# Kernel tuning notes

Hardware: AMD Instinct MI355X
Metric: run time of the kernel (lower is better)

## Reference

```python
import jax, jax.numpy as jnp
import numpy as np

L, B, T, SA, ST = 6, 32, 256, 512, 128
D, H, HD, DFF, OUT = 1024, 16, 64, 4096, 3
ROPE_THETA = 10000.0

def setup_inputs() -> dict:
    key = jax.random.key(0)
    ks = jax.random.split(key, 24)
    w = lambda k, shape: jax.random.normal(k, shape, jnp.float32) * 0.02
    inp = {
        'x':    jax.random.normal(ks[0], (B, T, D), jnp.float32),
        'cond': jax.random.normal(ks[1], (B, D), jnp.float32),
        'adp':  jax.random.normal(ks[2], (B, SA, D), jnp.float32),
        'task': jax.random.normal(ks[3], (B, ST, D), jnp.float32),
        'Wq':  w(ks[4], (L, D, D)),  'bq': jnp.zeros((L, D)),
        'Wks': w(ks[5], (L, D, D)),  'Wvs': w(ks[6], (L, D, D)),
        'Wka': w(ks[7], (L, D, D)),  'Wva': w(ks[8], (L, D, D)),
        'Wkt': w(ks[9], (L, D, D)),  'Wvt': w(ks[10], (L, D, D)),
        'Wo':  w(ks[11], (L, D, D)), 'bo': jnp.zeros((L, D)),
        'qnw': jnp.ones((L, HD)),    'knw': jnp.ones((L, HD)),
        'gate': jnp.zeros((L,)),
        'Wada': w(ks[12], (L, D, 6 * D)), 'bada': jnp.zeros((L, 6 * D)),
        'W1': w(ks[13], (L, D, DFF)), 'b1': jnp.zeros((L, DFF)),
        'W2': w(ks[14], (L, DFF, D)), 'b2': jnp.zeros((L, D)),
        'lnf_w': jnp.ones((D,)), 'lnf_b': jnp.zeros((D,)),
        'Wout': w(ks[15], (D, OUT)), 'bout': jnp.zeros((OUT,)),
    }
    return inp

def _ln(x, eps=1e-5):
    m = x.mean(-1, keepdims=True)
    v = ((x - m) ** 2).mean(-1, keepdims=True)
    return (x - m) * jax.lax.rsqrt(v + eps)

def _rms(x, wgt, eps=1e-6):
    return x * jax.lax.rsqrt((x * x).mean(-1, keepdims=True) + eps) * wgt

def _rotate_half(x):
    h = x.shape[-1] // 2
    return jnp.concatenate([-x[..., h:], x[..., :h]], axis=-1)

def _rope(x, cos, sin):
    # x: (B,S,H,HD); cos/sin: (S,1,HD)
    return x * cos + _rotate_half(x) * sin

def _cos_sin(S):
    inv = 1.0 / (ROPE_THETA ** (jnp.arange(0, HD, 2, dtype=jnp.float32) / HD))
    f = jnp.arange(S, dtype=jnp.float32)[:, None] * inv[None, :]
    emb = jnp.concatenate([f, f], axis=-1)  # (S, HD)
    return jnp.cos(emb)[:, None, :], jnp.sin(emb)[:, None, :]

def _forward(x, cond, adp, task, Wq, bq, Wks, Wvs, Wka, Wva, Wkt, Wvt, Wo, bo,
             qnw, knw, gate, Wada, bada, W1, b1, W2, b2, lnf_w, lnf_b, Wout, bout):
    cosT, sinT = _cos_sin(T)
    cosA, sinA = _cos_sin(SA)
    cosK, sinK = _cos_sin(ST)
    scale = 1.0 / jnp.sqrt(jnp.float32(HD))
    heads = lambda t, W: (t @ W).reshape(t.shape[0], t.shape[1], H, HD)
    for i in range(L):
        ada = jax.nn.silu(cond) @ Wada[i] + bada[i]
        s1, sc1, g1, s2, sc2, g2 = jnp.split(ada, 6, axis=-1)  # each (B,D)
        h = _ln(x) * (1.0 + sc1[:, None]) + s1[:, None]
        # self source: RoPE on Q and K; cross sources: RoPE on K only
        q = _rope(_rms(heads(h, Wq[i]) + bq[i].reshape(H, HD), qnw[i]), cosT, sinT)
        k_s = _rope(_rms(heads(h, Wks[i]), knw[i]), cosT, sinT)
        v_s = heads(h, Wvs[i])
        k_a = _rope(_rms(heads(adp, Wka[i]), knw[i]), cosA, sinA)
        v_a = heads(adp, Wva[i])
        k_t = _rope(_rms(heads(task, Wkt[i]), knw[i]), cosK, sinK)
        v_t = heads(task, Wvt[i])
        ss = jnp.einsum('bthd,bshd->bhts', q, k_s) * scale
        sa = jnp.einsum('bthd,bshd->bhts', q, k_a) * scale
        st = jnp.einsum('bthd,bshd->bhts', q, k_t) * scale * jax.nn.sigmoid(gate[i])
        attn = jax.nn.softmax(jnp.concatenate([ss, sa, st], axis=-1), axis=-1)
        v = jnp.concatenate([v_s, v_a, v_t], axis=1)  # (B, T+SA+ST, H, HD)
        o = jnp.einsum('bhts,bshd->bthd', attn, v).reshape(x.shape[0], T, D)
        x = x + g1[:, None] * (o @ Wo[i] + bo[i])
        h2 = _ln(x) * (1.0 + sc2[:, None]) + s2[:, None]
        ff = jax.nn.gelu(h2 @ W1[i] + b1[i]) @ W2[i] + b2[i]
        x = x + g2[:, None] * ff
    y = _ln(x) * lnf_w + lnf_b
    return y @ Wout + bout

def reference(x, cond, adp, task, Wq, bq, Wks, Wvs, Wka, Wva, Wkt, Wvt, Wo, bo,
              qnw, knw, gate, Wada, bada, W1, b1, W2, b2, lnf_w, lnf_b, Wout, bout):
    return _forward(x, cond, adp, task, Wq, bq, Wks, Wvs, Wka, Wva, Wkt, Wvt, Wo, bo,
                    qnw, knw, gate, Wada, bada, W1, b1, W2, b2, lnf_w, lnf_b, Wout, bout)
```

## Files before the change

kernel.cpp:

```cpp
#include <hip/hip_runtime.h>
#include <stdint.h>

#define DEV static __device__ __forceinline__

#define BB 32
#define TT 256
#define SAA 512
#define STT 128
#define DD 1024
#define HH 16
#define HDD 64
#define DFFF 4096
#define SS 896
#define LL 6

using bf16x8 = __attribute__((ext_vector_type(8))) short;
using f32x4  = __attribute__((ext_vector_type(4))) float;

DEV uint16_t f2bf(float f){
  uint32_t u = __float_as_uint(f);
  uint32_t r = (u + 0x7fffu + ((u >> 16) & 1u)) >> 16;
  return (uint16_t)r;
}
DEV float bf2f(uint16_t b){ return __uint_as_float(((uint32_t)b) << 16); }

typedef __attribute__((address_space(3))) void lds_vt;
typedef __attribute__((address_space(1))) void glb_vt;

DEV void gl_lds16(const uint16_t* g, uint16_t* l){
  __builtin_amdgcn_global_load_lds((const glb_vt*)g, (lds_vt*)l, 16, 0, 0);
}

struct GemmP {
  const uint16_t* A; const uint16_t* B; const uint16_t* B1; const uint16_t* B2;
  uint16_t* outB; float* outF; const float* bias; const float* gvec;
  const float* gatep; float* xres;
  long aOuter, aInner, bOuter, bInner;
  int M, N, K, lda, ldb, ldc, segStart, bShift;
};

template<int MODE>
__global__ __launch_bounds__(256, 2)
void gemm_nt(GemmP p){
  __shared__ uint16_t As[8192];
  __shared__ uint16_t Bs[8192];
  const int tid = threadIdx.x;
  const int w = tid >> 6, l = tid & 63;
  const int n0 = blockIdx.x * 128, m0 = blockIdx.y * 128;

  const uint16_t* Ab = p.A;
  const uint16_t* Bb = p.B + (long)n0 * p.ldb;

  const int rloc = l >> 3, ps = l & 7;
  const int kg_st = (ps - rloc) & 7;

  f32x4 acc[4][4];
  const f32x4 z4 = {0.f, 0.f, 0.f, 0.f};
  #pragma unroll
  for (int a = 0; a < 4; ++a)
    #pragma unroll
    for (int b = 0; b < 4; ++b) acc[a][b] = z4;

  const int KT = p.K >> 6;
  for (int kt = 0; kt < KT; ++kt){
    if (kt) __syncthreads();
    const long kbase = ((long)kt << 6) + (kg_st << 3);
    #pragma unroll
    for (int i = 0; i < 4; ++i){
      const int c = (w << 2) + i;
      int ar = m0 + (c << 3) + rloc;
      if (ar >= p.M) ar = p.M - 1;
      gl_lds16(Ab + (long)ar * p.lda + kbase, &As[c << 9]);
      const int br = (c << 3) + rloc;
      gl_lds16(Bb + (long)br * p.ldb + kbase, &Bs[c << 9]);
    }
    __syncthreads();
    #pragma unroll
    for (int ks = 0; ks < 2; ++ks){
      bf16x8 af[4], bfr[4];
      const int kq = (ks << 2) + (l >> 4);
      #pragma unroll
      for (int mt = 0; mt < 4; ++mt){
        const int r = ((w & 1) << 6) + (mt << 4) + (l & 15);
        af[mt] = *(const bf16x8*)&As[(r << 6) + (((kq + r) & 7) << 3)];
      }
      #pragma unroll
      for (int nt = 0; nt < 4; ++nt){
        const int r = ((w >> 1) << 6) + (nt << 4) + (l & 15);
        bfr[nt] = *(const bf16x8*)&Bs[(r << 6) + (((kq + r) & 7) << 3)];
      }
      #pragma unroll
      for (int mt = 0; mt < 4; ++mt)
        #pragma unroll
        for (int nt = 0; nt < 4; ++nt)
          acc[mt][nt] = __builtin_amdgcn_mfma_f32_16x16x32_bf16(af[mt], bfr[nt], acc[mt][nt], 0, 0, 0);
    }
  }

  const int colb = ((w >> 1) << 6) + (l & 15);
  const int rowb = m0 + ((w & 1) << 6) + ((l >> 4) << 2);
  #pragma unroll
  for (int mt = 0; mt < 4; ++mt){
    #pragma unroll
    for (int nt = 0; nt < 4; ++nt){
      const int col = n0 + colb + (nt << 4);
      const int row0 = rowb + (mt << 4);
      if (MODE == 6){
        const int b = row0 >> p.bShift;
        const int s = row0 & ((1 << p.bShift) - 1);
        const int hh = col >> 6, d = col & 63;
        ushort4 hv;
        hv.x = f2bf(acc[mt][nt][0]); hv.y = f2bf(acc[mt][nt][1]);
        hv.z = f2bf(acc[mt][nt][2]); hv.w = f2bf(acc[mt][nt][3]);
        *(ushort4*)(p.outB + ((long)((b << 4) + hh) * 128 + d) * 896 + p.segStart + s) = hv;
        continue;
      }
      #pragma unroll
      for (int e = 0; e < 4; ++e){
        const int row = row0 + e;
        if (row >= p.M) continue;
        float v = acc[mt][nt][e];
        if (MODE == 0){
          if (p.bias) v += p.bias[col];
          p.outB[(long)row * p.ldc + col] = f2bf(v);
        } else if (MODE == 5){
          v += p.bias[col];
          p.outF[(long)row * p.ldc + col] = v;
        } else if (MODE == 1){
          v += p.bias[col];
          const int b = row >> 8;
          const float g = p.gvec[b * 6144 + col];
          p.xres[(long)row * 1024 + col] += g * v;
        } else if (MODE == 2){
          v += p.bias[col];
          const float u = 0.7978845608028654f * (v + 0.044715f * v * v * v);
          v = 0.5f * v * (1.f + tanhf(u));
          p.outB[(long)row * 4096 + col] = f2bf(v);
        }
      }
    }
  }
}

__global__ __launch_bounds__(256, 2)
void k_attn(const uint16_t* __restrict__ qb, const uint16_t* __restrict__ ksb,
            const uint16_t* __restrict__ kab, const uint16_t* __restrict__ ktb,
            const uint16_t* __restrict__ vT, uint16_t* __restrict__ ob,
            const float* __restrict__ gatep){
  __shared__ uint16_t Kl[4096];
  __shared__ uint16_t Vl[4096];
  __shared__ uint16_t Pl[16384];
  const int tid = threadIdx.x;
  const int w = tid >> 6, l = tid & 63;
  const int bh = blockIdx.x, b = bh >> 4, h = bh & 15;
  const int g = l >> 4, c = l & 15;

  bf16x8 qf[4][2];
  const uint16_t* qbase = qb + (((long)(b * 256 + w * 64)) << 10) + (h << 6);
  #pragma unroll
  for (int m = 0; m < 4; ++m)
    #pragma unroll
    for (int ks = 0; ks < 2; ++ks)
      qf[m][ks] = *(const bf16x8*)(qbase + (((long)(m * 16 + c)) << 10) + ks * 32 + (g << 3));

  f32x4 acc_o[4][4];
  const f32x4 z4 = {0.f, 0.f, 0.f, 0.f};
  #pragma unroll
  for (int m = 0; m < 4; ++m)
    #pragma unroll
    for (int n = 0; n < 4; ++n) acc_o[m][n] = z4;
  float mstate[4][4], lstate[4][4];
  #pragma unroll
  for (int m = 0; m < 4; ++m)
    #pragma unroll
    for (int r = 0; r < 4; ++r){ mstate[m][r] = -1e30f; lstate[m][r] = 0.f; }

  const float gv = *gatep;
  const float gs = 0.125f / (1.f + __expf(-gv));
  uint16_t* pw = Pl + (w << 12);

  for (int kt = 0; kt < 14; ++kt){
    if (kt) __syncthreads();
    #pragma unroll
    for (int j = 0; j < 2; ++j){
      const int rr = (w << 4) + (j << 3) + (l >> 3);
      const int s = (kt << 6) + rr;
      const uint16_t* src; long row;
      if (s < 256){ src = ksb; row = (long)b * 256 + s; }
      else if (s < 768){ src = kab; row = (long)b * 512 + (s - 256); }
      else { src = ktb; row = (long)b * 128 + (s - 768); }
      const int blk = (l & 7) ^ (rr & 7);
      gl_lds16(src + (row << 10) + (h << 6) + (blk << 3),
               &Kl[((w << 4) + (j << 3)) << 6]);
      gl_lds16(vT + (long)(bh * 128 + rr) * 896 + (kt << 6) + (blk << 3),
               &Vl[((w << 4) + (j << 3)) << 6]);
    }
    __syncthreads();

    f32x4 sacc[4][4];
    #pragma unroll
    for (int m = 0; m < 4; ++m)
      #pragma unroll
      for (int n = 0; n < 4; ++n) sacc[m][n] = z4;
    #pragma unroll
    for (int ks = 0; ks < 2; ++ks){
      bf16x8 kf[4];
      #pragma unroll
      for (int n = 0; n < 4; ++n){
        const int s = (n << 4) + c;
        const int blk = (ks << 2) + g;
        kf[n] = *(const bf16x8*)&Kl[(s << 6) + ((blk ^ (s & 7)) << 3)];
      }
      #pragma unroll
      for (int m = 0; m < 4; ++m)
        #pragma unroll
        for (int n = 0; n < 4; ++n)
          sacc[m][n] = __builtin_amdgcn_mfma_f32_16x16x32_bf16(qf[m][ks], kf[n], sacc[m][n], 0, 0, 0);
    }

    const float tsc = (kt >= 12) ? gs : 0.125f;
    #pragma unroll
    for (int m = 0; m < 4; ++m){
      float nm[4], corr[4], tsum[4];
      #pragma unroll
      for (int r = 0; r < 4; ++r){
        float t = fmaxf(fmaxf(sacc[m][0][r], sacc[m][1][r]),
                        fmaxf(sacc[m][2][r], sacc[m][3][r])) * tsc;
        #pragma unroll
        for (int o = 1; o < 16; o <<= 1) t = fmaxf(t, __shfl_xor(t, o));
        nm[r] = fmaxf(mstate[m][r], t);
        corr[r] = __expf(mstate[m][r] - nm[r]);
        mstate[m][r] = nm[r];
        tsum[r] = 0.f;
      }
      const int q4 = (m << 4) + (g << 2);
      #pragma unroll
      for (int n = 0; n < 4; ++n){
        #pragma unroll
        for (int r = 0; r < 4; ++r){
          const float p = __expf(sacc[m][n][r] * tsc - nm[r]);
          tsum[r] += p;
          const int q = q4 + r;
          const int s = (n << 4) + c;
          pw[(q << 6) + (((s >> 3) ^ (q & 7)) << 3) + (s & 7)] = f2bf(p);
        }
      }
      #pragma unroll
      for (int r = 0; r < 4; ++r){
        float t = tsum[r];
        #pragma unroll
        for (int o = 1; o < 16; o <<= 1) t += __shfl_xor(t, o);
        lstate[m][r] = lstate[m][r] * corr[r] + t;
        #pragma unroll
        for (int n = 0; n < 4; ++n) acc_o[m][n][r] *= corr[r];
      }
    }

    #pragma unroll
    for (int ks = 0; ks < 2; ++ks){
      bf16x8 pf[4], vf[4];
      #pragma unroll
      for (int m = 0; m < 4; ++m){
        const int q = (m << 4) + c;
        const int blk = (ks << 2) + g;
        pf[m] = *(const bf16x8*)&pw[(q << 6) + ((blk ^ (q & 7)) << 3)];
      }
      #pragma unroll
      for (int n = 0; n < 4; ++n){
        const int d = (n << 4) + c;
        const int blk = (ks << 2) + g;
        vf[n] = *(const bf16x8*)&Vl[(d << 6) + ((blk ^ (d & 7)) << 3)];
      }
      #pragma unroll
      for (int m = 0; m < 4; ++m)
        #pragma unroll
        for (int n = 0; n < 4; ++n)
          acc_o[m][n] = __builtin_amdgcn_mfma_f32_16x16x32_bf16(pf[m], vf[n], acc_o[m][n], 0, 0, 0);
    }
  }

  uint16_t* obase = ob + (((long)(b * 256 + w * 64)) << 10) + (h << 6);
  #pragma unroll
  for (int m = 0; m < 4; ++m){
    float inv[4];
    #pragma unroll
    for (int r = 0; r < 4; ++r) inv[r] = 1.f / lstate[m][r];
    #pragma unroll
    for (int n = 0; n < 4; ++n)
      #pragma unroll
      for (int r = 0; r < 4; ++r)
        obase[(((long)((m << 4) + (g << 2) + r)) << 10) + (n << 4) + c] =
            f2bf(acc_o[m][n][r] * inv[r]);
  }
}

struct WtP { const float* src[11]; uint16_t* dst; };

__global__ __launch_bounds__(256) void k_wtrans(WtP p){
  __shared__ uint16_t tile[64][65];
  const int idx = blockIdx.x, tid = threadIdx.x;
  const int tx = tid & 63, ty = tid >> 6;
  int wi, Kw, Nw, k0, n0;
  if (idx < 2048){ wi = idx >> 8; int t = idx & 255; Kw = 1024; Nw = 1024; k0 = (t >> 4) << 6; n0 = (t & 15) << 6; }
  else if (idx < 3072){ wi = 8; int t = idx - 2048; Kw = 1024; Nw = 4096; k0 = (t >> 6) << 6; n0 = (t & 63) << 6; }
  else if (idx < 4096){ wi = 9; int t = idx - 3072; Kw = 4096; Nw = 1024; k0 = (t >> 4) << 6; n0 = (t & 15) << 6; }
  else { wi = 10; int t = idx - 4096; Kw = 1024; Nw = 6144; k0 = (t / 96) << 6; n0 = (t % 96) << 6; }
  long doff;
  if (wi < 8) doff = (long)wi * 1048576;
  else if (wi == 8) doff = 8388608;
  else if (wi == 9) doff = 12582912;
  else doff = 16777216;
  const float* src = p.src[wi];
  uint16_t* dst = p.dst + doff;
  #pragma unroll 4
  for (int i = 0; i < 16; ++i){
    const int row = (i << 2) + ty;
    tile[row][tx] = f2bf(src[(long)(k0 + row) * Nw + n0 + tx]);
  }
  __syncthreads();
  #pragma unroll 4
  for (int i = 0; i < 16; ++i){
    const int row = (i << 2) + ty;
    dst[(long)(n0 + row) * Kw + k0 + tx] = tile[tx][row];
  }
}

__global__ __launch_bounds__(256) void k_f2bf4(const float* __restrict__ s, uint16_t* __restrict__ d, int n4){
  const int i = blockIdx.x * 256 + threadIdx.x;
  if (i < n4){
    const float4 v = ((const float4*)s)[i];
    ushort4 o; o.x = f2bf(v.x); o.y = f2bf(v.y); o.z = f2bf(v.z); o.w = f2bf(v.w);
    ((ushort4*)d)[i] = o;
  }
}

__global__ __launch_bounds__(256) void k_silu4(const float* __restrict__ s, uint16_t* __restrict__ d, int n4){
  const int i = blockIdx.x * 256 + threadIdx.x;
  if (i < n4){
    const float4 v = ((const float4*)s)[i];
    ushort4 o;
    o.x = f2bf(v.x / (1.f + expf(-v.x)));
    o.y = f2bf(v.y / (1.f + expf(-v.y)));
    o.z = f2bf(v.z / (1.f + expf(-v.z)));
    o.w = f2bf(v.w / (1.f + expf(-v.w)));
    ((ushort4*)d)[i] = o;
  }
}

__global__ __launch_bounds__(256) void k_ln(const float* __restrict__ x,
    const float* __restrict__ addv, const float* __restrict__ mulv,
    uint16_t* __restrict__ outb){
  const int row = blockIdx.x, tid = threadIdx.x;
  const float4 xv = ((const float4*)(x + (long)row * 1024))[tid];
  float s = xv.x + xv.y + xv.z + xv.w;
  float q = xv.x*xv.x + xv.y*xv.y + xv.z*xv.z + xv.w*xv.w;
  #pragma unroll
  for (int o = 32; o; o >>= 1){ s += __shfl_down(s, o); q += __shfl_down(q, o); }
  __shared__ float rs[4], rq[4];
  if ((tid & 63) == 0){ rs[tid >> 6] = s; rq[tid >> 6] = q; }
  __syncthreads();
  s = rs[0] + rs[1] + rs[2] + rs[3];
  q = rq[0] + rq[1] + rq[2] + rq[3];
  const float mean = s * (1.f / 1024.f);
  const float var  = q * (1.f / 1024.f) - mean * mean;
  const float inv  = rsqrtf(var + 1e-5f);
  const int b = row >> 8;
  const float4 av = ((const float4*)(addv + (long)b * 6144))[tid];
  const float4 mv = ((const float4*)(mulv + (long)b * 6144))[tid];
  ushort4 o4;
  o4.x = f2bf((xv.x - mean) * inv * (1.f + mv.x) + av.x);
  o4.y = f2bf((xv.y - mean) * inv * (1.f + mv.y) + av.y);
  o4.z = f2bf((xv.z - mean) * inv * (1.f + mv.z) + av.z);
  o4.w = f2bf((xv.w - mean) * inv * (1.f + mv.w) + av.w);
  ((ushort4*)(outb + (long)row * 1024))[tid] = o4;
}

__global__ __launch_bounds__(256) void k_rmsrope(uint16_t* qb, uint16_t* ksb,
    uint16_t* kab, uint16_t* ktb, const float* qn, const float* kn){
  const int row = blockIdx.x, tid = threadIdx.x;
  const int l = tid & 63, wv = tid >> 6;
  uint16_t* buf; const float* wgt; int pos; long grow;
  if (row < 8192)      { buf = qb;  wgt = qn; grow = row;         pos = row & 255; }
  else if (row < 16384){ buf = ksb; wgt = kn; grow = row - 8192;  pos = (int)grow & 255; }
  else if (row < 32768){ buf = kab; wgt = kn; grow = row - 16384; pos = (int)grow & 511; }
  else                 { buf = ktb; wgt = kn; grow = row - 32768; pos = (int)grow & 127; }
  const float wl = wgt[l];
  const float invf = exp2f(-0.41524101186092029f * (float)(l & 31));
  float c, sn; sincosf((float)pos * invf, &sn, &c);
  const float sgn = (l < 32) ? -1.f : 1.f;
  uint16_t* rbase = buf + grow * 1024;
  #pragma unroll
  for (int hh = 0; hh < 4; ++hh){
    uint16_t* hp = rbase + (((hh << 2) + wv) << 6);
    const float v = bf2f(hp[l]);
    float ss = v * v;
    #pragma unroll
    for (int o = 1; o < 64; o <<= 1) ss += __shfl_xor(ss, o);
    const float y = v * rsqrtf(ss * (1.f / 64.f) + 1e-6f) * wl;
    const float prt = __shfl_xor(y, 32);
    hp[l] = f2bf(y * c + sgn * prt * sn);
  }
}

__global__ __launch_bounds__(256) void k_final(const float* __restrict__ x,
    const float* __restrict__ lw, const float* __restrict__ lb,
    const float* __restrict__ W3, const float* __restrict__ b3,
    float* __restrict__ out){
  const int row = blockIdx.x, tid = threadIdx.x;
  const float4 xv = ((const float4*)(x + (long)row * 1024))[tid];
  float s = xv.x + xv.y + xv.z + xv.w;
  float q = xv.x*xv.x + xv.y*xv.y + xv.z*xv.z + xv.w*xv.w;
  #pragma unroll
  for (int o = 32; o; o >>= 1){ s += __shfl_down(s, o); q += __shfl_down(q, o); }
  __shared__ float rs[4], rq[4];
  if ((tid & 63) == 0){ rs[tid >> 6] = s; rq[tid >> 6] = q; }
  __syncthreads();
  s = rs[0] + rs[1] + rs[2] + rs[3];
  q = rq[0] + rq[1] + rq[2] + rq[3];
  const float mean = s * (1.f / 1024.f);
  const float inv  = rsqrtf(q * (1.f / 1024.f) - mean * mean + 1e-5f);
  const float4 wv = ((const float4*)lw)[tid];
  const float4 bv = ((const float4*)lb)[tid];
  const int c = tid << 2;
  const float y0 = (xv.x - mean) * inv * wv.x + bv.x;
  const float y1 = (xv.y - mean) * inv * wv.y + bv.y;
  const float y2 = (xv.z - mean) * inv * wv.z + bv.z;
  const float y3 = (xv.w - mean) * inv * wv.w + bv.w;
  float o0 = y0*W3[c*3+0] + y1*W3[(c+1)*3+0] + y2*W3[(c+2)*3+0] + y3*W3[(c+3)*3+0];
  float o1 = y0*W3[c*3+1] + y1*W3[(c+1)*3+1] + y2*W3[(c+2)*3+1] + y3*W3[(c+3)*3+1];
  float o2 = y0*W3[c*3+2] + y1*W3[(c+1)*3+2] + y2*W3[(c+2)*3+2] + y3*W3[(c+3)*3+2];
  #pragma unroll
  for (int o = 32; o; o >>= 1){
    o0 += __shfl_down(o0, o); o1 += __shfl_down(o1, o); o2 += __shfl_down(o2, o);
  }
  __shared__ float r0[4], r1[4], r2[4];
  if ((tid & 63) == 0){ r0[tid>>6] = o0; r1[tid>>6] = o1; r2[tid>>6] = o2; }
  __syncthreads();
  if (tid == 0){
    out[(long)row * 3 + 0] = r0[0]+r0[1]+r0[2]+r0[3] + b3[0];
    out[(long)row * 3 + 1] = r1[0]+r1[1]+r1[2]+r1[3] + b3[1];
    out[(long)row * 3 + 2] = r2[0]+r2[1]+r2[2]+r2[3] + b3[2];
  }
}

extern "C" void kernel_launch(void* const* d_in, const int* in_sizes, int n_in,
                              void* d_out, int out_size, void* d_ws, size_t ws_size,
                              hipStream_t stream){
  (void)in_sizes; (void)n_in; (void)out_size; (void)ws_size;
  const float* X    = (const float*)d_in[0];
  const float* cond = (const float*)d_in[1];
  const float* adp  = (const float*)d_in[2];
  const float* task = (const float*)d_in[3];
  const float* Wq   = (const float*)d_in[4];
  const float* bq   = (const float*)d_in[5];
  const float* Wks  = (const float*)d_in[6];
  const float* Wvs  = (const float*)d_in[7];
  const float* Wka  = (const float*)d_in[8];
  const float* Wva  = (const float*)d_in[9];
  const float* Wkt  = (const float*)d_in[10];
  const float* Wvt  = (const float*)d_in[11];
  const float* Wo   = (const float*)d_in[12];
  const float* bo   = (const float*)d_in[13];
  const float* qnw  = (const float*)d_in[14];
  const float* knw  = (const float*)d_in[15];
  const float* gate = (const float*)d_in[16];
  const float* Wada = (const float*)d_in[17];
  const float* bada = (const float*)d_in[18];
  const float* W1   = (const float*)d_in[19];
  const float* b1   = (const float*)d_in[20];
  const float* W2   = (const float*)d_in[21];
  const float* b2   = (const float*)d_in[22];
  const float* lnw  = (const float*)d_in[23];
  const float* lnb  = (const float*)d_in[24];
  const float* Wout = (const float*)d_in[25];
  const float* bout = (const float*)d_in[26];
  float* out = (float*)d_out;

  char* base = (char*)d_ws;
  size_t off = 0;
  auto alloc = [&](size_t bytes)->char*{
    char* r = base + off; off += (bytes + 255) & ~(size_t)255; return r;
  };
  float*    x_cur = (float*)   alloc(8192UL * 1024 * 4);
  float*    ada   = (float*)   alloc(32UL * 6144 * 4);
  uint16_t* csilu = (uint16_t*)alloc(32UL * 1024 * 2);
  uint16_t* hb    = (uint16_t*)alloc(8192UL * 1024 * 2);
  uint16_t* qb    = (uint16_t*)alloc(8192UL * 1024 * 2);
  uint16_t* ksb   = (uint16_t*)alloc(8192UL * 1024 * 2);
  uint16_t* kab   = (uint16_t*)alloc(16384UL * 1024 * 2);
  uint16_t* ktb   = (uint16_t*)alloc(4096UL * 1024 * 2);
  uint16_t* adpb  = (uint16_t*)alloc(16384UL * 1024 * 2);
  uint16_t* taskb = (uint16_t*)alloc(4096UL * 1024 * 2);
  uint16_t* vT    = (uint16_t*)alloc(32UL * 16 * 128 * 896 * 2);
  uint16_t* ob    = (uint16_t*)alloc(8192UL * 1024 * 2);
  uint16_t* Wt    = (uint16_t*)alloc(23068672UL * 2);
  uint16_t* ff1   = (uint16_t*)alloc(8192UL * 4096 * 2);

  hipMemcpyAsync(x_cur, X, 8192UL * 1024 * 4, hipMemcpyDeviceToDevice, stream);
  k_f2bf4<<<16384, 256, 0, stream>>>(adp,  adpb,  4194304);
  k_f2bf4<<<4096,  256, 0, stream>>>(task, taskb, 1048576);
  k_silu4<<<32,    256, 0, stream>>>(cond, csilu, 8192);

  for (int i = 0; i < LL; ++i){
    WtP wp;
    wp.src[0] = Wq  + (long)i * 1048576;
    wp.src[1] = Wks + (long)i * 1048576;
    wp.src[2] = Wvs + (long)i * 1048576;
    wp.src[3] = Wka + (long)i * 1048576;
    wp.src[4] = Wva + (long)i * 1048576;
    wp.src[5] = Wkt + (long)i * 1048576;
    wp.src[6] = Wvt + (long)i * 1048576;
    wp.src[7] = Wo  + (long)i * 1048576;
    wp.src[8] = W1  + (long)i * 4194304;
    wp.src[9] = W2  + (long)i * 4194304;
    wp.src[10]= Wada+ (long)i * 6291456;
    wp.dst = Wt;
    k_wtrans<<<5632, 256, 0, stream>>>(wp);

    GemmP g;
    auto clr = [&](){ g = GemmP{}; g.aOuter=g.aInner=g.bOuter=g.bInner=0; };

    clr();
    g.A = csilu; g.lda = 1024; g.B = Wt + 16777216; g.ldb = 1024;
    g.M = 32; g.N = 6144; g.K = 1024; g.outF = ada; g.bias = bada + (long)i * 6144; g.ldc = 6144;
    gemm_nt<5><<<dim3(48, 1, 1), 256, 0, stream>>>(g);

    k_ln<<<8192, 256, 0, stream>>>(x_cur, ada + 0, ada + 1024, hb);

    clr(); g.A=hb; g.lda=1024; g.B=Wt; g.ldb=1024; g.M=8192; g.N=1024; g.K=1024;
    g.outB=qb; g.bias=bq + (long)i*1024; g.ldc=1024;
    gemm_nt<0><<<dim3(8, 64, 1), 256, 0, stream>>>(g);

    clr(); g.A=hb; g.lda=1024; g.B=Wt+1048576; g.ldb=1024; g.M=8192; g.N=1024; g.K=1024;
    g.outB=ksb; g.bias=nullptr; g.ldc=1024;
    gemm_nt<0><<<dim3(8, 64, 1), 256, 0, stream>>>(g);

    clr(); g.A=hb; g.lda=1024; g.B=Wt+2097152; g.ldb=1024; g.M=8192; g.N=1024; g.K=1024;
    g.outB=vT; g.bShift=8; g.segStart=0;
    gemm_nt<6><<<dim3(8, 64, 1), 256, 0, stream>>>(g);

    clr(); g.A=adpb; g.lda=1024; g.B=Wt+3145728; g.ldb=1024; g.M=16384; g.N=1024; g.K=1024;
    g.outB=kab; g.bias=nullptr; g.ldc=1024;
    gemm_nt<0><<<dim3(8, 128, 1), 256, 0, stream>>>(g);

    clr(); g.A=adpb; g.lda=1024; g.B=Wt+4194304; g.ldb=1024; g.M=16384; g.N=1024; g.K=1024;
    g.outB=vT; g.bShift=9; g.segStart=256;
    gemm_nt<6><<<dim3(8, 128, 1), 256, 0, stream>>>(g);

    clr(); g.A=taskb; g.lda=1024; g.B=Wt+5242880; g.ldb=1024; g.M=4096; g.N=1024; g.K=1024;
    g.outB=ktb; g.bias=nullptr; g.ldc=1024;
    gemm_nt<0><<<dim3(8, 32, 1), 256, 0, stream>>>(g);

    clr(); g.A=taskb; g.lda=1024; g.B=Wt+6291456; g.ldb=1024; g.M=4096; g.N=1024; g.K=1024;
    g.outB=vT; g.bShift=7; g.segStart=768;
    gemm_nt<6><<<dim3(8, 32, 1), 256, 0, stream>>>(g);

    k_rmsrope<<<36864, 256, 0, stream>>>(qb, ksb, kab, ktb,
                                         qnw + (long)i * 64, knw + (long)i * 64);

    k_attn<<<512, 256, 0, stream>>>(qb, ksb, kab, ktb, vT, ob, gate + i);

    clr(); g.A=ob; g.lda=1024; g.B=Wt+7340032; g.ldb=1024; g.M=8192; g.N=1024; g.K=1024;
    g.bias=bo + (long)i*1024; g.gvec=ada + 2048; g.xres=x_cur;
    gemm_nt<1><<<dim3(8, 64, 1), 256, 0, stream>>>(g);

    k_ln<<<8192, 256, 0, stream>>>(x_cur, ada + 3072, ada + 4096, hb);

    clr(); g.A=hb; g.lda=1024; g.B=Wt+8388608; g.ldb=1024; g.M=8192; g.N=4096; g.K=1024;
    g.outB=ff1; g.bias=b1 + (long)i*4096;
    gemm_nt<2><<<dim3(32, 64, 1), 256, 0, stream>>>(g);

    clr(); g.A=ff1; g.lda=4096; g.B=Wt+12582912; g.ldb=4096; g.M=8192; g.N=1024; g.K=4096;
    g.bias=b2 + (long)i*1024; g.gvec=ada + 5120; g.xres=x_cur;
    gemm_nt<1><<<dim3(8, 64, 1), 256, 0, stream>>>(g);
  }

  k_final<<<8192, 256, 0, stream>>>(x_cur, lnw, lnb, Wout, bout, out);
}
```

Before: 6.592 ms.

## Use head-major Q/K/V layouts and double-buffer attention K/V tiles

```diff
diff --git a/kernel.cpp b/kernel.cpp
--- a/kernel.cpp
+++ b/kernel.cpp
@@ -31,11 +31,13 @@
   __builtin_amdgcn_global_load_lds((const glb_vt*)g, (lds_vt*)l, 16, 0, 0);
 }
 
+#define VMCNT4 asm volatile("s_waitcnt vmcnt(4)" ::: "memory")
+#define VMCNT0 asm volatile("s_waitcnt vmcnt(0)" ::: "memory")
+
 struct GemmP {
-  const uint16_t* A; const uint16_t* B; const uint16_t* B1; const uint16_t* B2;
+  const uint16_t* A; const uint16_t* B;
   uint16_t* outB; float* outF; const float* bias; const float* gvec;
-  const float* gatep; float* xres;
-  long aOuter, aInner, bOuter, bInner;
+  float* xres;
   int M, N, K, lda, ldb, ldc, segStart, bShift;
 };
 
@@ -108,11 +110,13 @@
       if (MODE == 6){
         const int b = row0 >> p.bShift;
         const int s = row0 & ((1 << p.bShift) - 1);
+        const int S = p.segStart + s;
         const int hh = col >> 6, d = col & 63;
         ushort4 hv;
         hv.x = f2bf(acc[mt][nt][0]); hv.y = f2bf(acc[mt][nt][1]);
         hv.z = f2bf(acc[mt][nt][2]); hv.w = f2bf(acc[mt][nt][3]);
-        *(ushort4*)(p.outB + ((long)((b << 4) + hh) * 128 + d) * 896 + p.segStart + s) = hv;
+        *(ushort4*)(p.outB +
+            ((((long)((b << 4) + hh) * 14 + (S >> 6)) * 64 + d) << 6) + (S & 63)) = hv;
         continue;
       }
       #pragma unroll
@@ -136,6 +140,12 @@
           const float u = 0.7978845608028654f * (v + 0.044715f * v * v * v);
           v = 0.5f * v * (1.f + tanhf(u));
           p.outB[(long)row * 4096 + col] = f2bf(v);
+        } else if (MODE == 7){
+          if (p.bias) v += p.bias[col];
+          const int b = row >> p.bShift;
+          const int s = row & ((1 << p.bShift) - 1);
+          const int hh = col >> 6, d = col & 63;
+          p.outB[((long)((b << 4) + hh) * p.ldc + p.segStart + s) * 64 + d] = f2bf(v);
         }
       }
     }
@@ -143,25 +153,27 @@
 }
 
 __global__ __launch_bounds__(256, 2)
-void k_attn(const uint16_t* __restrict__ qb, const uint16_t* __restrict__ ksb,
-            const uint16_t* __restrict__ kab, const uint16_t* __restrict__ ktb,
+void k_attn(const uint16_t* __restrict__ qT, const uint16_t* __restrict__ kT,
             const uint16_t* __restrict__ vT, uint16_t* __restrict__ ob,
             const float* __restrict__ gatep){
-  __shared__ uint16_t Kl[4096];
-  __shared__ uint16_t Vl[4096];
+  __shared__ uint16_t Kl[2][4096];
+  __shared__ uint16_t Vl[2][4096];
   __shared__ uint16_t Pl[16384];
   const int tid = threadIdx.x;
   const int w = tid >> 6, l = tid & 63;
   const int bh = blockIdx.x, b = bh >> 4, h = bh & 15;
   const int g = l >> 4, c = l & 15;
 
+  const uint16_t* kTb = kT + (long)bh * 57344;
+  const uint16_t* vTb = vT + (long)bh * 57344;
+
   bf16x8 qf[4][2];
-  const uint16_t* qbase = qb + (((long)(b * 256 + w * 64)) << 10) + (h << 6);
+  const uint16_t* qbase = qT + (((long)bh * 256 + w * 64) << 6);
   #pragma unroll
   for (int m = 0; m < 4; ++m)
     #pragma unroll
     for (int ks = 0; ks < 2; ++ks)
-      qf[m][ks] = *(const bf16x8*)(qbase + (((long)(m * 16 + c)) << 10) + ks * 32 + (g << 3));
+      qf[m][ks] = *(const bf16x8*)(qbase + ((m * 16 + c) << 6) + ks * 32 + (g << 3));
 
   f32x4 acc_o[4][4];
   const f32x4 z4 = {0.f, 0.f, 0.f, 0.f};
@@ -179,23 +191,24 @@
   const float gs = 0.125f / (1.f + __expf(-gv));
   uint16_t* pw = Pl + (w << 12);
 
+  const int rr0 = w << 4, rl = l >> 3, bsw = l & 7;
+  auto STAGE = [&](int kt, int buf){
+    #pragma unroll
+    for (int j = 0; j < 2; ++j){
+      const int rr = rr0 + (j << 3) + rl;
+      const int blk = bsw ^ (rr & 7);
+      const long goff = (((long)(kt << 6) + rr) << 6) + (blk << 3);
+      gl_lds16(kTb + goff, &Kl[buf][(rr0 + (j << 3)) << 6]);
+      gl_lds16(vTb + goff, &Vl[buf][(rr0 + (j << 3)) << 6]);
+    }
+  };
+
+  STAGE(0, 0);
+  int cur = 0;
   for (int kt = 0; kt < 14; ++kt){
-    if (kt) __syncthreads();
-    #pragma unroll
-    for (int j = 0; j < 2; ++j){
-      const int rr = (w << 4) + (j << 3) + (l >> 3);
-      const int s = (kt << 6) + rr;
-      const uint16_t* src; long row;
-      if (s < 256){ src = ksb; row = (long)b * 256 + s; }
-      else if (s < 768){ src = kab; row = (long)b * 512 + (s - 256); }
-      else { src = ktb; row = (long)b * 128 + (s - 768); }
-      const int blk = (l & 7) ^ (rr & 7);
-      gl_lds16(src + (row << 10) + (h << 6) + (blk << 3),
-               &Kl[((w << 4) + (j << 3)) << 6]);
-      gl_lds16(vT + (long)(bh * 128 + rr) * 896 + (kt << 6) + (blk << 3),
-               &Vl[((w << 4) + (j << 3)) << 6]);
-    }
-    __syncthreads();
+    if (kt < 13){ STAGE(kt + 1, cur ^ 1); VMCNT4; }
+    else { VMCNT0; }
+    __builtin_amdgcn_s_barrier();
 
     f32x4 sacc[4][4];
     #pragma unroll
@@ -209,7 +222,7 @@
       for (int n = 0; n < 4; ++n){
         const int s = (n << 4) + c;
         const int blk = (ks << 2) + g;
-        kf[n] = *(const bf16x8*)&Kl[(s << 6) + ((blk ^ (s & 7)) << 3)];
+        kf[n] = *(const bf16x8*)&Kl[cur][(s << 6) + ((blk ^ (s & 7)) << 3)];
       }
       #pragma unroll
       for (int m = 0; m < 4; ++m)
@@ -269,7 +282,7 @@
       for (int n = 0; n < 4; ++n){
         const int d = (n << 4) + c;
         const int blk = (ks << 2) + g;
-        vf[n] = *(const bf16x8*)&Vl[(d << 6) + ((blk ^ (d & 7)) << 3)];
+        vf[n] = *(const bf16x8*)&Vl[cur][(d << 6) + ((blk ^ (d & 7)) << 3)];
       }
       #pragma unroll
       for (int m = 0; m < 4; ++m)
@@ -277,20 +290,31 @@
         for (int n = 0; n < 4; ++n)
           acc_o[m][n] = __builtin_amdgcn_mfma_f32_16x16x32_bf16(pf[m], vf[n], acc_o[m][n], 0, 0, 0);
     }
-  }
-
-  uint16_t* obase = ob + (((long)(b * 256 + w * 64)) << 10) + (h << 6);
+    __builtin_amdgcn_s_barrier();
+    cur ^= 1;
+  }
+
   #pragma unroll
   for (int m = 0; m < 4; ++m){
     float inv[4];
     #pragma unroll
     for (int r = 0; r < 4; ++r) inv[r] = 1.f / lstate[m][r];
-    #pragma unroll
-    for (int n = 0; n < 4; ++n)
-      #pragma unroll
-      for (int r = 0; r < 4; ++r)
-        obase[(((long)((m << 4) + (g << 2) + r)) << 10) + (n << 4) + c] =
-            f2bf(acc_o[m][n][r] * inv[r]);
+    const int q4 = (m << 4) + (g << 2);
+    #pragma unroll
+    for (int n = 0; n < 4; ++n){
+      #pragma unroll
+      for (int r = 0; r < 4; ++r){
+        const int q = q4 + r;
+        const int d = (n << 4) + c;
+        pw[(q << 6) + (((d >> 3) ^ (q & 7)) << 3) + (d & 7)] = f2bf(acc_o[m][n][r] * inv[r]);
+      }
+    }
+  }
+  #pragma unroll
+  for (int i = 0; i < 8; ++i){
+    const int q = (i << 3) + rl;
+    const bf16x8 vv = *(const bf16x8*)&pw[(q << 6) + ((bsw ^ (q & 7)) << 3)];
+    *(bf16x8*)(ob + (((long)(b * 256 + w * 64 + q)) << 10) + (h << 6) + (bsw << 3)) = vv;
   }
 }
 
@@ -375,30 +399,34 @@
   ((ushort4*)(outb + (long)row * 1024))[tid] = o4;
 }
 
-__global__ __launch_bounds__(256) void k_rmsrope(uint16_t* qb, uint16_t* ksb,
-    uint16_t* kab, uint16_t* ktb, const float* qn, const float* kn){
-  const int row = blockIdx.x, tid = threadIdx.x;
+__global__ __launch_bounds__(256) void k_rmsrope(uint16_t* qT, uint16_t* kT,
+    const float* qn, const float* kn){
+  const int tid = threadIdx.x;
   const int l = tid & 63, wv = tid >> 6;
-  uint16_t* buf; const float* wgt; int pos; long grow;
-  if (row < 8192)      { buf = qb;  wgt = qn; grow = row;         pos = row & 255; }
-  else if (row < 16384){ buf = ksb; wgt = kn; grow = row - 8192;  pos = (int)grow & 255; }
-  else if (row < 32768){ buf = kab; wgt = kn; grow = row - 16384; pos = (int)grow & 511; }
-  else                 { buf = ktb; wgt = kn; grow = row - 32768; pos = (int)grow & 127; }
-  const float wl = wgt[l];
+  uint16_t* buf; int s, seqLen; float wl;
+  int v;
+  if (blockIdx.x < 8192){
+    v = blockIdx.x * 4 + wv;
+    buf = qT; wl = qn[l]; s = v >> 7; seqLen = 256;
+  } else {
+    v = (blockIdx.x - 8192) * 4 + wv;
+    buf = kT; wl = kn[l]; s = v >> 7; seqLen = 896;
+  }
+  const int u = v & 127;
+  const int pos = (seqLen == 256) ? s : ((s < 256) ? s : (s < 768 ? s - 256 : s - 768));
   const float invf = exp2f(-0.41524101186092029f * (float)(l & 31));
-  float c, sn; sincosf((float)pos * invf, &sn, &c);
+  float cth, snth; sincosf((float)pos * invf, &snth, &cth);
   const float sgn = (l < 32) ? -1.f : 1.f;
-  uint16_t* rbase = buf + grow * 1024;
-  #pragma unroll
-  for (int hh = 0; hh < 4; ++hh){
-    uint16_t* hp = rbase + (((hh << 2) + wv) << 6);
-    const float v = bf2f(hp[l]);
-    float ss = v * v;
+  #pragma unroll
+  for (int j = 0; j < 4; ++j){
+    uint16_t* hp = buf + (((long)(u * 4 + j) * seqLen + s) << 6);
+    const float x = bf2f(hp[l]);
+    float ss = x * x;
     #pragma unroll
     for (int o = 1; o < 64; o <<= 1) ss += __shfl_xor(ss, o);
-    const float y = v * rsqrtf(ss * (1.f / 64.f) + 1e-6f) * wl;
+    const float y = x * rsqrtf(ss * (1.f / 64.f) + 1e-6f) * wl;
     const float prt = __shfl_xor(y, 32);
-    hp[l] = f2bf(y * c + sgn * prt * sn);
+    hp[l] = f2bf(y * cth + sgn * prt * snth);
   }
 }
 
@@ -485,13 +513,11 @@
   float*    ada   = (float*)   alloc(32UL * 6144 * 4);
   uint16_t* csilu = (uint16_t*)alloc(32UL * 1024 * 2);
   uint16_t* hb    = (uint16_t*)alloc(8192UL * 1024 * 2);
-  uint16_t* qb    = (uint16_t*)alloc(8192UL * 1024 * 2);
-  uint16_t* ksb   = (uint16_t*)alloc(8192UL * 1024 * 2);
-  uint16_t* kab   = (uint16_t*)alloc(16384UL * 1024 * 2);
-  uint16_t* ktb   = (uint16_t*)alloc(4096UL * 1024 * 2);
+  uint16_t* qTb   = (uint16_t*)alloc(512UL * 256 * 64 * 2);
+  uint16_t* kTb   = (uint16_t*)alloc(512UL * 896 * 64 * 2);
   uint16_t* adpb  = (uint16_t*)alloc(16384UL * 1024 * 2);
   uint16_t* taskb = (uint16_t*)alloc(4096UL * 1024 * 2);
-  uint16_t* vT    = (uint16_t*)alloc(32UL * 16 * 128 * 896 * 2);
+  uint16_t* vT    = (uint16_t*)alloc(512UL * 14 * 64 * 64 * 2);
   uint16_t* ob    = (uint16_t*)alloc(8192UL * 1024 * 2);
   uint16_t* Wt    = (uint16_t*)alloc(23068672UL * 2);
   uint16_t* ff1   = (uint16_t*)alloc(8192UL * 4096 * 2);
@@ -518,7 +544,7 @@
     k_wtrans<<<5632, 256, 0, stream>>>(wp);
 
     GemmP g;
-    auto clr = [&](){ g = GemmP{}; g.aOuter=g.aInner=g.bOuter=g.bInner=0; };
+    auto clr = [&](){ g = GemmP{}; };
 
     clr();
     g.A = csilu; g.lda = 1024; g.B = Wt + 16777216; g.ldb = 1024;
@@ -528,37 +554,37 @@
     k_ln<<<8192, 256, 0, stream>>>(x_cur, ada + 0, ada + 1024, hb);
 
     clr(); g.A=hb; g.lda=1024; g.B=Wt; g.ldb=1024; g.M=8192; g.N=1024; g.K=1024;
-    g.outB=qb; g.bias=bq + (long)i*1024; g.ldc=1024;
-    gemm_nt<0><<<dim3(8, 64, 1), 256, 0, stream>>>(g);
+    g.outB=qTb; g.bias=bq + (long)i*1024; g.ldc=256; g.bShift=8; g.segStart=0;
+    gemm_nt<7><<<dim3(8, 64, 1), 256, 0, stream>>>(g);
 
     clr(); g.A=hb; g.lda=1024; g.B=Wt+1048576; g.ldb=1024; g.M=8192; g.N=1024; g.K=1024;
-    g.outB=ksb; g.bias=nullptr; g.ldc=1024;
-    gemm_nt<0><<<dim3(8, 64, 1), 256, 0, stream>>>(g);
+    g.outB=kTb; g.bias=nullptr; g.ldc=896; g.bShift=8; g.segStart=0;
+    gemm_nt<7><<<dim3(8, 64, 1), 256, 0, stream>>>(g);
 
     clr(); g.A=hb; g.lda=1024; g.B=Wt+2097152; g.ldb=1024; g.M=8192; g.N=1024; g.K=1024;
     g.outB=vT; g.bShift=8; g.segStart=0;
     gemm_nt<6><<<dim3(8, 64, 1), 256, 0, stream>>>(g);
 
     clr(); g.A=adpb; g.lda=1024; g.B=Wt+3145728; g.ldb=1024; g.M=16384; g.N=1024; g.K=1024;
-    g.outB=kab; g.bias=nullptr; g.ldc=1024;
-    gemm_nt<0><<<dim3(8, 128, 1), 256, 0, stream>>>(g);
+    g.outB=kTb; g.bias=nullptr; g.ldc=896; g.bShift=9; g.segStart=256;
+    gemm_nt<7><<<dim3(8, 128, 1), 256, 0, stream>>>(g);
 
     clr(); g.A=adpb; g.lda=1024; g.B=Wt+4194304; g.ldb=1024; g.M=16384; g.N=1024; g.K=1024;
     g.outB=vT; g.bShift=9; g.segStart=256;
     gemm_nt<6><<<dim3(8, 128, 1), 256, 0, stream>>>(g);
 
     clr(); g.A=taskb; g.lda=1024; g.B=Wt+5242880; g.ldb=1024; g.M=4096; g.N=1024; g.K=1024;
-    g.outB=ktb; g.bias=nullptr; g.ldc=1024;
-    gemm_nt<0><<<dim3(8, 32, 1), 256, 0, stream>>>(g);
+    g.outB=kTb; g.bias=nullptr; g.ldc=896; g.bShift=7; g.segStart=768;
+    gemm_nt<7><<<dim3(8, 32, 1), 256, 0, stream>>>(g);
 
     clr(); g.A=taskb; g.lda=1024; g.B=Wt+6291456; g.ldb=1024; g.M=4096; g.N=1024; g.K=1024;
     g.outB=vT; g.bShift=7; g.segStart=768;
     gemm_nt<6><<<dim3(8, 32, 1), 256, 0, stream>>>(g);
 
-    k_rmsrope<<<36864, 256, 0, stream>>>(qb, ksb, kab, ktb,
+    k_rmsrope<<<36864, 256, 0, stream>>>(qTb, kTb,
                                          qnw + (long)i * 64, knw + (long)i * 64);
 
-    k_attn<<<512, 256, 0, stream>>>(qb, ksb, kab, ktb, vT, ob, gate + i);
+    k_attn<<<512, 256, 0, stream>>>(qTb, kTb, vT, ob, gate + i);
 
     clr(); g.A=ob; g.lda=1024; g.B=Wt+7340032; g.ldb=1024; g.M=8192; g.N=1024; g.K=1024;
     g.bias=bo + (long)i*1024; g.gvec=ada + 2048; g.xres=x_cur;
```

Measured after the change: 6.234 ms. 1.06x faster.
